# Performance work log

Measured on AMD Instinct MI355X. Metric: run time of the kernel, lower is better.

Reference implementation:

```python
import jax, jax.numpy as jnp
import numpy as np

B, H, W, C = 8, 64, 64, 256
EPS = 1e-5


def unfold(img, k, p):
    # img: [B, C, Hh, Ww] -> patches [B, C, k*k, Hh*Ww] (torch.nn.Unfold layout)
    b, c, hh, ww = img.shape
    xp = jnp.pad(img, ((0, 0), (0, 0), (p, p), (p, p)))
    pats = jnp.stack([xp[:, :, i:i + hh, j:j + ww]
                      for i in range(k) for j in range(k)], axis=2)
    return pats.reshape(b, c, k * k, hh * ww)


def fold(cols, k, p, hh, ww):
    # cols: [B, C*k*k, hh*ww] -> scatter-add back to [B, C, hh, ww] (torch.nn.Fold)
    b = cols.shape[0]
    c = cols.shape[1] // (k * k)
    pt = cols.reshape(b, c, k, k, hh, ww)
    out = jnp.zeros((b, c, hh + 2 * p, ww + 2 * p), cols.dtype)
    for i in range(k):
        for j in range(k):
            out = out.at[:, :, i:i + hh, j:j + ww].add(pt[:, :, i, j])
    return out[:, :, p:p + hh, p:p + ww]


def maxpool(img, k, p):
    # same-size max pool, stride 1
    return jax.lax.reduce_window(img, -jnp.inf, jax.lax.max,
                                 (1, 1, k, k), (1, 1, 1, 1),
                                 [(0, 0), (0, 0), (p, p), (p, p)])


def setup_inputs() -> dict:
    key = jax.random.key(0)
    ks = jax.random.split(key, 4)
    x = jax.random.normal(ks[0], (B, H, W, C), dtype=jnp.float32)
    Wv = jax.random.normal(ks[1], (C, C), dtype=jnp.float32) * 0.02
    bv = jnp.zeros((C,), jnp.float32)
    Wa = jax.random.normal(ks[2], (C, 81), dtype=jnp.float32) * 0.02
    ba = jnp.zeros((81,), jnp.float32)
    Wfu = jax.random.normal(ks[3], (2 * C, C), dtype=jnp.float32) * 0.02
    bfu = jnp.zeros((C,), jnp.float32)
    gamma = jnp.ones((C,), jnp.float32)
    beta = jnp.zeros((C,), jnp.float32)
    return {"x": x, "Wv": Wv, "bv": bv, "Wa": Wa, "ba": ba,
            "Wfu": Wfu, "bfu": bfu, "gamma": gamma, "beta": beta}


def reference(x, Wv, bv, Wa, ba, Wfu, bfu, gamma, beta):
    b, h, w, c = x.shape
    x3 = x
    # 3x3 windowed attention branch (5x5 branch in source is dead code: its
    # result is overwritten by `x2 = relu(x)` before use).
    v = x @ Wv + bv                                # [B,H,W,C]
    v_img = jnp.transpose(v, (0, 3, 2, 1))         # [B,C,W,H] (H/W swap as in source)
    pats = unfold(v_img, 3, 1)                     # [B,C,9,W*H]
    v3 = jnp.transpose(pats, (0, 3, 2, 1))         # [B,HW,9,C]
    a = (x @ Wa + ba).reshape(b, h * w, 9, 9)
    a = jax.nn.softmax(a, axis=-1)
    y = jnp.einsum('lbpq,lbqc->lbpc'.replace('l', 'n'), a, v3)  # [B,HW,9,C]
    y = jnp.transpose(y, (0, 3, 2, 1)).reshape(b, c * 9, h * w)
    xf = fold(y, 3, 1, h, w)                       # [B,C,H,W]
    xf = jnp.transpose(xf, (0, 3, 2, 1))           # [B,W,H,C]
    xr = jax.nn.relu(xf)
    x_max = jnp.transpose(x3, (0, 3, 2, 1))        # [B,C,W,H]
    m1 = jnp.transpose(maxpool(x_max, 3, 1), (0, 3, 2, 1))  # [B,H,W,C]
    x1 = jax.nn.relu(xr + m1)
    x2 = jax.nn.relu(x1)
    m2 = jnp.transpose(maxpool(x_max, 5, 2), (0, 3, 2, 1))
    x2 = jax.nn.relu(x2 + m2)
    xfu = jnp.concatenate([x1, x2], axis=-1) @ Wfu + bfu
    xfu = jax.nn.relu(xfu)
    out = x3 + xfu                                 # [B,H,W,C]
    # BatchNorm2d (training mode: batch stats) applied on [B,C,W,H]
    img = jnp.transpose(out, (0, 3, 2, 1))
    mean = img.mean(axis=(0, 2, 3), keepdims=True)
    var = img.var(axis=(0, 2, 3), keepdims=True)
    imgn = (img - mean) * jax.lax.rsqrt(var + EPS)
    imgn = imgn * gamma[None, :, None, None] + beta[None, :, None, None]
    return jnp.transpose(imgn, (0, 2, 3, 1))       # [B,W,H,C]
```

## Files before the change

kernel.cpp:

```cpp
#include <hip/hip_runtime.h>
#include <math.h>

#define NLOC 32768
#define CH 256

typedef __attribute__((ext_vector_type(8))) short short8;
typedef __attribute__((ext_vector_type(4))) float floatx4;

__device__ inline unsigned short f2bf(float x) {
  union { float f; unsigned u; } c; c.f = x;
  unsigned r = c.u + 0x7FFFu + ((c.u >> 16) & 1u);
  return (unsigned short)(r >> 16);
}
__device__ inline float bflo(unsigned u) {
  union { unsigned u; float f; } c; c.u = u << 16; return c.f;
}
__device__ inline float bfhi(unsigned u) {
  union { unsigned u; float f; } c; c.u = u & 0xFFFF0000u; return c.f;
}

__device__ __forceinline__ void gl_lds16(const void* g, void* l) {
  __builtin_amdgcn_global_load_lds(
      (const __attribute__((address_space(1))) unsigned int*)g,
      (__attribute__((address_space(3))) unsigned int*)l, 16, 0, 0);
}

__global__ __launch_bounds__(64) void k_pack_w(
    const float* __restrict__ Wv, const float* __restrict__ Wa,
    const float* __restrict__ Wfu, unsigned short* __restrict__ wp) {
  int fid = blockIdx.x;
  int l = threadIdx.x;
  const float* W; int ldn, nvalid, nf, ks;
  if (fid < 128)      { W = Wv;  ldn = 256; nvalid = 256; nf = fid >> 3; ks = fid & 7; }
  else if (fid < 384) { int f = fid - 128; W = Wfu; ldn = 256; nvalid = 256; nf = f >> 4; ks = f & 15; }
  else                { int f = fid - 384; W = Wa;  ldn = 81;  nvalid = 81;  nf = f >> 3; ks = f & 7; }
  unsigned short* dst = wp + (size_t)fid * 512;
  int c = nf * 16 + (l & 15);
  int k0 = ks * 32 + (l >> 4) * 8;
  unsigned short u[8];
#pragma unroll
  for (int j = 0; j < 8; ++j)
    u[j] = (c < nvalid) ? f2bf(W[(size_t)(k0 + j) * ldn + c]) : (unsigned short)0;
  uint4 pk;
  pk.x = u[0] | ((unsigned)u[1] << 16);
  pk.y = u[2] | ((unsigned)u[3] << 16);
  pk.z = u[4] | ((unsigned)u[5] << 16);
  pk.w = u[6] | ((unsigned)u[7] << 16);
  *(uint4*)(dst + l * 8) = pk;
}

__global__ __launch_bounds__(256) void k_pool(
    const float* __restrict__ x, unsigned short* __restrict__ rm3,
    unsigned short* __restrict__ rm5, unsigned short* __restrict__ xb) {
  int tid = threadIdx.x;
  int loc = blockIdx.x * 4 + (tid >> 6);
  int beta = loc & 63;
  int c0 = (tid & 63) * 4;
  const float* base = x + ((size_t)loc - beta) * CH + c0;
  const float NI = -INFINITY;
  float4 r3 = {NI, NI, NI, NI}, r5, xv;
#pragma unroll
  for (int d = -1; d <= 1; ++d) {
    int bb = beta + d;
    if ((unsigned)bb >= 64u) continue;
    float4 f = *(const float4*)(base + (size_t)bb * CH);
    if (d == 0) xv = f;
    r3.x = fmaxf(r3.x, f.x); r3.y = fmaxf(r3.y, f.y);
    r3.z = fmaxf(r3.z, f.z); r3.w = fmaxf(r3.w, f.w);
  }
  r5 = r3;
#pragma unroll
  for (int d = -2; d <= 2; d += 4) {
    int bb = beta + d;
    if ((unsigned)bb >= 64u) continue;
    float4 f = *(const float4*)(base + (size_t)bb * CH);
    r5.x = fmaxf(r5.x, f.x); r5.y = fmaxf(r5.y, f.y);
    r5.z = fmaxf(r5.z, f.z); r5.w = fmaxf(r5.w, f.w);
  }
  size_t o = (size_t)loc * CH + c0;
  uint2 p3, p5, px;
  p3.x = f2bf(r3.x) | ((unsigned)f2bf(r3.y) << 16);
  p3.y = f2bf(r3.z) | ((unsigned)f2bf(r3.w) << 16);
  p5.x = f2bf(r5.x) | ((unsigned)f2bf(r5.y) << 16);
  p5.y = f2bf(r5.z) | ((unsigned)f2bf(r5.w) << 16);
  px.x = f2bf(xv.x) | ((unsigned)f2bf(xv.y) << 16);
  px.y = f2bf(xv.z) | ((unsigned)f2bf(xv.w) << 16);
  *(uint2*)(rm3 + o) = p3;
  *(uint2*)(rm5 + o) = p5;
  *(uint2*)(xb + o) = px;
}

__global__ __launch_bounds__(256) void k_gemm_v(
    const unsigned short* __restrict__ xb, const unsigned short* __restrict__ wvp,
    const float* __restrict__ bv, unsigned short* __restrict__ v) {
  __shared__ unsigned short sA[16 * 512];
  __shared__ unsigned short sB[16 * 512];
  int tid = threadIdx.x, lane = tid & 63, w = tid >> 6;
  int r0 = (blockIdx.x >> 1) * 128;
  int nc0 = (blockIdx.x & 1) * 128;
  int mh = w >> 1, nq = w & 1;
  floatx4 acc[4][4];
#pragma unroll
  for (int mt = 0; mt < 4; ++mt)
#pragma unroll
    for (int nf = 0; nf < 4; ++nf) acc[mt][nf] = (floatx4)(0.f);
  for (int kt = 0; kt < 4; ++kt) {
    int kk = kt * 64;
#pragma unroll
    for (int f = 0; f < 4; ++f) {
      int fa = w * 4 + f;
      int mt = fa >> 1, ks = fa & 1;
      const unsigned short* g = xb + (size_t)(r0 + mt * 16 + (lane & 15)) * CH
                                + kk + ks * 32 + (lane >> 4) * 8;
      gl_lds16(g, &sA[fa * 512]);
    }
#pragma unroll
    for (int f = 0; f < 4; ++f) {
      int fb = w * 4 + f;
      int nf = fb >> 1, ks = fb & 1;
      int nfg = (nc0 >> 4) + nf;
      int ksg = kt * 2 + ks;
      const unsigned short* g = wvp + ((size_t)nfg * 8 + ksg) * 512 + lane * 8;
      gl_lds16(g, &sB[fb * 512]);
    }
    __syncthreads();
#pragma unroll
    for (int ks = 0; ks < 2; ++ks) {
      short8 af[4], bf[4];
#pragma unroll
      for (int mt = 0; mt < 4; ++mt)
        af[mt] = *(const short8*)&sA[(((mh * 4 + mt) << 1) + ks) * 512 + lane * 8];
#pragma unroll
      for (int nf = 0; nf < 4; ++nf)
        bf[nf] = *(const short8*)&sB[(((nq * 4 + nf) << 1) + ks) * 512 + lane * 8];
#pragma unroll
      for (int mt = 0; mt < 4; ++mt)
#pragma unroll
        for (int nf = 0; nf < 4; ++nf)
          acc[mt][nf] = __builtin_amdgcn_mfma_f32_16x16x32_bf16(af[mt], bf[nf], acc[mt][nf], 0, 0, 0);
    }
    if (kt < 3) __syncthreads();
  }
#pragma unroll
  for (int nf = 0; nf < 4; ++nf) {
    int c = nc0 + nq * 64 + nf * 16 + (lane & 15);
    float bb = bv[c];
#pragma unroll
    for (int mt = 0; mt < 4; ++mt) {
      int crow = r0 + mh * 64 + mt * 16 + (lane >> 4) * 4;
#pragma unroll
      for (int i = 0; i < 4; ++i)
        v[(size_t)(crow + i) * CH + c] = f2bf(acc[mt][nf][i] + bb);
    }
  }
}

__global__ __launch_bounds__(256) void k_gemm_a(
    const unsigned short* __restrict__ xb, const unsigned short* __restrict__ wap,
    const float* __restrict__ ba, float* __restrict__ A) {
  __shared__ float lg[64][96];
  int tid = threadIdx.x, lane = tid & 63, w = tid >> 6;
  int mtile = blockIdx.x * 4 + w;
  int r0 = mtile * 16;
  floatx4 acc[6];
#pragma unroll
  for (int i = 0; i < 6; ++i) acc[i] = (floatx4)(0.f);
  const unsigned short* abase = xb + (size_t)(r0 + (lane & 15)) * CH + (lane >> 4) * 8;
  for (int ks = 0; ks < 8; ++ks) {
    short8 af = *(const short8*)(abase + ks * 32);
#pragma unroll
    for (int nf = 0; nf < 6; ++nf) {
      short8 bfr = *(const short8*)(wap + ((size_t)(nf * 8) + ks) * 512 + lane * 8);
      acc[nf] = __builtin_amdgcn_mfma_f32_16x16x32_bf16(af, bfr, acc[nf], 0, 0, 0);
    }
  }
  int lrow = w * 16 + (lane >> 4) * 4;
#pragma unroll
  for (int nf = 0; nf < 6; ++nf) {
    int c = nf * 16 + (lane & 15);
    float bb = (c < 81) ? ba[c] : 0.f;
#pragma unroll
    for (int i = 0; i < 4; ++i)
      lg[lrow + i][c] = acc[nf][i] + bb;
  }
  __syncthreads();
  int loc0 = blockIdx.x * 64;
  for (int it = 0; it < 3; ++it) {
    int idx = tid + it * 256;
    if (idx < 576) {
      int row = idx / 9, g = idx % 9;
      float vals[9];
#pragma unroll
      for (int q = 0; q < 9; ++q) vals[q] = lg[row][g * 9 + q];
      float m = vals[0];
#pragma unroll
      for (int q = 1; q < 9; ++q) m = fmaxf(m, vals[q]);
      float s = 0.f;
#pragma unroll
      for (int q = 0; q < 9; ++q) { vals[q] = __expf(vals[q] - m); s += vals[q]; }
      float inv = 1.f / s;
      float* o = A + (size_t)(loc0 + row) * 81 + g * 9;
#pragma unroll
      for (int q = 0; q < 9; ++q) o[q] = vals[q] * inv;
    }
  }
}

__global__ __launch_bounds__(256) void k_attn(
    const float* __restrict__ A, const unsigned short* __restrict__ v,
    const unsigned short* __restrict__ rm3, const unsigned short* __restrict__ rm5,
    unsigned short* __restrict__ cat) {
  __shared__ unsigned short vs[5 * 12 * CH];
  __shared__ float w5_s[8][25];
  float* a_sf = (float*)vs;
  int tid = threadIdx.x;
  int loc0 = blockIdx.x * 8;
  int b = loc0 >> 12, alpha = (loc0 >> 6) & 63, beta0 = loc0 & 63;
  for (int idx = tid; idx < 8 * 81; idx += 256) {
    int li = idx / 81, t = idx - li * 81;
    int ij = t / 9, i = ij / 3, j = ij % 3;
    int lh = beta0 + li + 1 - i;
    int lw = alpha + 1 - j;
    float val = 0.f;
    if ((unsigned)lh < 64u && (unsigned)lw < 64u)
      val = A[(size_t)(b * 4096 + lh * 64 + lw) * 81 + t];
    a_sf[li * 81 + t] = val;
  }
  __syncthreads();
  for (int idx = tid; idx < 200; idx += 256) {
    int li = idx / 25, o = idx - li * 25;
    int dh = o / 5 - 2, dw = o % 5 - 2;
    float s = 0.f;
    int jlo = dh < 0 ? -dh : 0, jhi = dh > 0 ? 2 - dh : 2;
    int ilo = dw < 0 ? -dw : 0, ihi = dw > 0 ? 2 - dw : 2;
    for (int j = jlo; j <= jhi; ++j)
      for (int i = ilo; i <= ihi; ++i)
        s += a_sf[li * 81 + (i * 3 + j) * 9 + ((i + dw) * 3 + (j + dh))];
    w5_s[li][o] = s;
  }
  __syncthreads();
  const unsigned short* vb = v + (size_t)b * 4096 * CH;
  for (int i = tid; i < 1920; i += 256) {
    int row = i / 384, rem = i - row * 384, col = rem >> 5, ch8 = rem & 31;
    int hv = alpha - 2 + row, wv = beta0 - 2 + col;
    uint4 val = {0u, 0u, 0u, 0u};
    if ((unsigned)hv < 64u && (unsigned)wv < 64u)
      val = *(const uint4*)(vb + (size_t)(hv * 64 + wv) * CH + ch8 * 8);
    *(uint4*)(vs + (size_t)(row * 12 + col) * CH + ch8 * 8) = val;
  }
  __syncthreads();
  int li = tid >> 5, tc = tid & 31, c0 = tc * 8;
  int beta = beta0 + li;
  float m1[8], m2[8];
#pragma unroll
  for (int q = 0; q < 8; ++q) { m1[q] = -INFINITY; m2[q] = -INFINITY; }
#pragma unroll
  for (int da = -2; da <= 2; ++da) {
    int aa = alpha + da;
    if ((unsigned)aa >= 64u) continue;
    size_t ro = (size_t)((b * 64 + aa) * 64 + beta) * CH + c0;
    uint4 p5 = *(const uint4*)(rm5 + ro);
    m2[0] = fmaxf(m2[0], bflo(p5.x)); m2[1] = fmaxf(m2[1], bfhi(p5.x));
    m2[2] = fmaxf(m2[2], bflo(p5.y)); m2[3] = fmaxf(m2[3], bfhi(p5.y));
    m2[4] = fmaxf(m2[4], bflo(p5.z)); m2[5] = fmaxf(m2[5], bfhi(p5.z));
    m2[6] = fmaxf(m2[6], bflo(p5.w)); m2[7] = fmaxf(m2[7], bfhi(p5.w));
    if (da >= -1 && da <= 1) {
      uint4 p3 = *(const uint4*)(rm3 + ro);
      m1[0] = fmaxf(m1[0], bflo(p3.x)); m1[1] = fmaxf(m1[1], bfhi(p3.x));
      m1[2] = fmaxf(m1[2], bflo(p3.y)); m1[3] = fmaxf(m1[3], bfhi(p3.y));
      m1[4] = fmaxf(m1[4], bflo(p3.z)); m1[5] = fmaxf(m1[5], bfhi(p3.z));
      m1[6] = fmaxf(m1[6], bflo(p3.w)); m1[7] = fmaxf(m1[7], bfhi(p3.w));
    }
  }
  float acc[8];
#pragma unroll
  for (int q = 0; q < 8; ++q) acc[q] = 0.f;
#pragma unroll
  for (int dh = 0; dh < 5; ++dh) {
#pragma unroll
    for (int dw = 0; dw < 5; ++dw) {
      float wgt = w5_s[li][dh * 5 + dw];
      uint4 pk = *(const uint4*)(vs + (size_t)(dh * 12 + li + dw) * CH + c0);
      acc[0] = fmaf(wgt, bflo(pk.x), acc[0]);
      acc[1] = fmaf(wgt, bfhi(pk.x), acc[1]);
      acc[2] = fmaf(wgt, bflo(pk.y), acc[2]);
      acc[3] = fmaf(wgt, bfhi(pk.y), acc[3]);
      acc[4] = fmaf(wgt, bflo(pk.z), acc[4]);
      acc[5] = fmaf(wgt, bfhi(pk.z), acc[5]);
      acc[6] = fmaf(wgt, bflo(pk.w), acc[6]);
      acc[7] = fmaf(wgt, bfhi(pk.w), acc[7]);
    }
  }
  unsigned short u1[8], u2[8];
#pragma unroll
  for (int q = 0; q < 8; ++q) {
    float x1v = fmaxf(fmaxf(acc[q], 0.f) + m1[q], 0.f);
    float x2v = fmaxf(x1v + m2[q], 0.f);
    u1[q] = f2bf(x1v);
    u2[q] = f2bf(x2v);
  }
  unsigned short* cp = cat + (size_t)(loc0 + li) * 512 + c0;
  uint4 pk1, pk2;
  pk1.x = u1[0] | ((unsigned)u1[1] << 16); pk1.y = u1[2] | ((unsigned)u1[3] << 16);
  pk1.z = u1[4] | ((unsigned)u1[5] << 16); pk1.w = u1[6] | ((unsigned)u1[7] << 16);
  pk2.x = u2[0] | ((unsigned)u2[1] << 16); pk2.y = u2[2] | ((unsigned)u2[3] << 16);
  pk2.z = u2[4] | ((unsigned)u2[5] << 16); pk2.w = u2[6] | ((unsigned)u2[7] << 16);
  *(uint4*)(cp) = pk1;
  *(uint4*)(cp + 256) = pk2;
}

__global__ __launch_bounds__(256) void k_fuse(
    const float* __restrict__ x, const unsigned short* __restrict__ cat,
    const unsigned short* __restrict__ wfp, const float* __restrict__ bfu,
    float* __restrict__ outp, float* __restrict__ sums16) {
  __shared__ unsigned short sA[16 * 512];
  __shared__ unsigned short sB[16 * 512];
  __shared__ float bsum[512];
  int tid = threadIdx.x, lane = tid & 63, w = tid >> 6;
  for (int i = tid; i < 512; i += 256) bsum[i] = 0.f;
  int r0 = (blockIdx.x >> 1) * 128;
  int nc0 = (blockIdx.x & 1) * 128;
  int mh = w >> 1, nq = w & 1;
  floatx4 acc[4][4];
#pragma unroll
  for (int mt = 0; mt < 4; ++mt)
#pragma unroll
    for (int nf = 0; nf < 4; ++nf) acc[mt][nf] = (floatx4)(0.f);
  for (int kt = 0; kt < 8; ++kt) {
    int kk = kt * 64;
#pragma unroll
    for (int f = 0; f < 4; ++f) {
      int fa = w * 4 + f;
      int mt = fa >> 1, ks = fa & 1;
      const unsigned short* g = cat + (size_t)(r0 + mt * 16 + (lane & 15)) * 512
                                + kk + ks * 32 + (lane >> 4) * 8;
      gl_lds16(g, &sA[fa * 512]);
    }
#pragma unroll
    for (int f = 0; f < 4; ++f) {
      int fb = w * 4 + f;
      int nf = fb >> 1, ks = fb & 1;
      int nfg = (nc0 >> 4) + nf;
      int ksg = kt * 2 + ks;
      const unsigned short* g = wfp + ((size_t)nfg * 16 + ksg) * 512 + lane * 8;
      gl_lds16(g, &sB[fb * 512]);
    }
    __syncthreads();
#pragma unroll
    for (int ks = 0; ks < 2; ++ks) {
      short8 af[4], bf[4];
#pragma unroll
      for (int mt = 0; mt < 4; ++mt)
        af[mt] = *(const short8*)&sA[(((mh * 4 + mt) << 1) + ks) * 512 + lane * 8];
#pragma unroll
      for (int nf = 0; nf < 4; ++nf)
        bf[nf] = *(const short8*)&sB[(((nq * 4 + nf) << 1) + ks) * 512 + lane * 8];
#pragma unroll
      for (int mt = 0; mt < 4; ++mt)
#pragma unroll
        for (int nf = 0; nf < 4; ++nf)
          acc[mt][nf] = __builtin_amdgcn_mfma_f32_16x16x32_bf16(af[mt], bf[nf], acc[mt][nf], 0, 0, 0);
    }
    if (kt < 7) __syncthreads();
  }
#pragma unroll
  for (int nf = 0; nf < 4; ++nf) {
    int c = nc0 + nq * 64 + nf * 16 + (lane & 15);
    float bb = bfu[c];
    float s = 0.f, ss = 0.f;
#pragma unroll
    for (int mt = 0; mt < 4; ++mt) {
      int crow = r0 + mh * 64 + mt * 16 + (lane >> 4) * 4;
#pragma unroll
      for (int i = 0; i < 4; ++i) {
        int r = crow + i;
        float xv = x[(size_t)r * CH + c];
        float o = xv + fmaxf(acc[mt][nf][i] + bb, 0.f);
        int b_ = r >> 12, al = (r >> 6) & 63, be = r & 63;
        outp[((size_t)(b_ * 64 + be) * 64 + al) * CH + c] = o;
        s += o; ss += o * o;
      }
    }
    s += __shfl_xor(s, 16);  s += __shfl_xor(s, 32);
    ss += __shfl_xor(ss, 16); ss += __shfl_xor(ss, 32);
    if (lane < 16) {
      atomicAdd(&bsum[c & 255], s);
      atomicAdd(&bsum[256 + (c & 255)], ss);
    }
  }
  __syncthreads();
  float* bank = sums16 + (size_t)(blockIdx.x & 15) * 512;
  for (int i = tid; i < 512; i += 256) atomicAdd(&bank[i], bsum[i]);
}

__global__ void k_bnprep(const float* __restrict__ sums16,
                         const float* __restrict__ gamma,
                         const float* __restrict__ beta_,
                         float* __restrict__ sc) {
  int c = threadIdx.x;
  float s = 0.f, ss = 0.f;
#pragma unroll
  for (int bk = 0; bk < 16; ++bk) {
    s += sums16[(size_t)bk * 512 + c];
    ss += sums16[(size_t)bk * 512 + 256 + c];
  }
  const float inv_n = 1.f / (float)NLOC;
  float mean = s * inv_n;
  float var = ss * inv_n - mean * mean;
  float scale = gamma[c] * rsqrtf(var + 1e-5f);
  sc[c] = scale;
  sc[256 + c] = beta_[c] - mean * scale;
}

__global__ __launch_bounds__(256) void k_bn(
    float* __restrict__ outp, const float* __restrict__ sc, int n4) {
  __shared__ float s[512];
  const int tid = threadIdx.x;
  for (int i = tid; i < 512; i += 256) s[i] = sc[i];
  __syncthreads();
  for (int i = blockIdx.x * 256 + tid; i < n4; i += gridDim.x * 256) {
    float4 val = ((float4*)outp)[i];
    int c0 = (i & 63) * 4;
    val.x = val.x * s[c0 + 0] + s[256 + c0 + 0];
    val.y = val.y * s[c0 + 1] + s[256 + c0 + 1];
    val.z = val.z * s[c0 + 2] + s[256 + c0 + 2];
    val.w = val.w * s[c0 + 3] + s[256 + c0 + 3];
    ((float4*)outp)[i] = val;
  }
}

extern "C" void kernel_launch(void* const* d_in, const int* in_sizes, int n_in,
                              void* d_out, int out_size, void* d_ws, size_t ws_size,
                              hipStream_t stream) {
  const float* x     = (const float*)d_in[0];
  const float* Wv    = (const float*)d_in[1];
  const float* bv    = (const float*)d_in[2];
  const float* Wa    = (const float*)d_in[3];
  const float* ba    = (const float*)d_in[4];
  const float* Wfu   = (const float*)d_in[5];
  const float* bfu   = (const float*)d_in[6];
  const float* gamma = (const float*)d_in[7];
  const float* beta_ = (const float*)d_in[8];
  float* out = (float*)d_out;

  float* sums16 = (float*)d_ws;
  float* sc   = sums16 + 16 * 512;
  unsigned short* wp   = (unsigned short*)(sc + 512);
  unsigned short* wvp  = wp;
  unsigned short* wfp  = wp + (size_t)128 * 512;
  unsigned short* wap  = wp + (size_t)384 * 512;
  unsigned short* vbuf = wp + (size_t)432 * 512;
  float* Abuf = (float*)(vbuf + (size_t)NLOC * CH);
  unsigned short* cat = (unsigned short*)(Abuf + (size_t)NLOC * 81);
  unsigned short* rm3 = cat + (size_t)NLOC * 512;
  unsigned short* rm5 = rm3 + (size_t)NLOC * CH;
  unsigned short* xb  = rm5 + (size_t)NLOC * CH;

  hipMemsetAsync(sums16, 0, 16 * 512 * sizeof(float), stream);

  k_pack_w<<<432, 64, 0, stream>>>(Wv, Wa, Wfu, wp);
  k_pool<<<8192, 256, 0, stream>>>(x, rm3, rm5, xb);
  k_gemm_v<<<512, 256, 0, stream>>>(xb, wvp, bv, vbuf);
  k_gemm_a<<<512, 256, 0, stream>>>(xb, wap, ba, Abuf);
  k_attn<<<4096, 256, 0, stream>>>(Abuf, vbuf, rm3, rm5, cat);
  k_fuse<<<512, 256, 0, stream>>>(x, cat, wfp, bfu, out, sums16);
  k_bnprep<<<1, 256, 0, stream>>>(sums16, gamma, beta_, sc);
  k_bn<<<2048, 256, 0, stream>>>(out, sc, NLOC * CH / 4);
}
```

Measured before the change: 131.7 us.

## Double-buffer LDS tiles in both GEMMs and widen attention blocks to 512 threads

Both bf16 MFMA GEMM kernels now keep two LDS stages and issue the global-to-LDS loads for the next K tile before computing on the current one, so load latency can overlap with the MFMA work. LDS use per block doubles, which may lower occupancy. Separately, the attention kernel runs with 512 threads per block, each handling 4 channels instead of 8, to give more parallelism per location. This halves the width of each vector access and adds more threads to the staging loops.

```diff
diff --git a/kernel.cpp b/kernel.cpp
--- a/kernel.cpp
+++ b/kernel.cpp
@@ -93,8 +93,8 @@
 __global__ __launch_bounds__(256) void k_gemm_v(
     const unsigned short* __restrict__ xb, const unsigned short* __restrict__ wvp,
     const float* __restrict__ bv, unsigned short* __restrict__ v) {
-  __shared__ unsigned short sA[16 * 512];
-  __shared__ unsigned short sB[16 * 512];
+  __shared__ unsigned short sA[2][16 * 512];
+  __shared__ unsigned short sB[2][16 * 512];
   int tid = threadIdx.x, lane = tid & 63, w = tid >> 6;
   int r0 = (blockIdx.x >> 1) * 128;
   int nc0 = (blockIdx.x & 1) * 128;
@@ -104,42 +104,46 @@
   for (int mt = 0; mt < 4; ++mt)
 #pragma unroll
     for (int nf = 0; nf < 4; ++nf) acc[mt][nf] = (floatx4)(0.f);
+#pragma unroll
+  for (int f = 0; f < 4; ++f) {
+    int fa = w * 4 + f, mt = fa >> 1, ks = fa & 1;
+    gl_lds16(xb + (size_t)(r0 + mt * 16 + (lane & 15)) * CH + ks * 32 + (lane >> 4) * 8,
+             &sA[0][fa * 512]);
+    int fb = fa, nf = fb >> 1;
+    gl_lds16(wvp + ((size_t)((nc0 >> 4) + nf) * 8 + ks) * 512 + lane * 8,
+             &sB[0][fb * 512]);
+  }
+  __syncthreads();
   for (int kt = 0; kt < 4; ++kt) {
-    int kk = kt * 64;
-#pragma unroll
-    for (int f = 0; f < 4; ++f) {
-      int fa = w * 4 + f;
-      int mt = fa >> 1, ks = fa & 1;
-      const unsigned short* g = xb + (size_t)(r0 + mt * 16 + (lane & 15)) * CH
-                                + kk + ks * 32 + (lane >> 4) * 8;
-      gl_lds16(g, &sA[fa * 512]);
-    }
-#pragma unroll
-    for (int f = 0; f < 4; ++f) {
-      int fb = w * 4 + f;
-      int nf = fb >> 1, ks = fb & 1;
-      int nfg = (nc0 >> 4) + nf;
-      int ksg = kt * 2 + ks;
-      const unsigned short* g = wvp + ((size_t)nfg * 8 + ksg) * 512 + lane * 8;
-      gl_lds16(g, &sB[fb * 512]);
-    }
-    __syncthreads();
+    int cur = kt & 1;
+    if (kt < 3) {
+      int kn = kt + 1, nb = kn & 1, kkn = kn * 64;
+#pragma unroll
+      for (int f = 0; f < 4; ++f) {
+        int fa = w * 4 + f, mt = fa >> 1, ks = fa & 1;
+        gl_lds16(xb + (size_t)(r0 + mt * 16 + (lane & 15)) * CH + kkn + ks * 32 + (lane >> 4) * 8,
+                 &sA[nb][fa * 512]);
+        int fb = fa, nf = fb >> 1;
+        gl_lds16(wvp + ((size_t)((nc0 >> 4) + nf) * 8 + kn * 2 + ks) * 512 + lane * 8,
+                 &sB[nb][fb * 512]);
+      }
+    }
 #pragma unroll
     for (int ks = 0; ks < 2; ++ks) {
       short8 af[4], bf[4];
 #pragma unroll
       for (int mt = 0; mt < 4; ++mt)
-        af[mt] = *(const short8*)&sA[(((mh * 4 + mt) << 1) + ks) * 512 + lane * 8];
+        af[mt] = *(const short8*)&sA[cur][(((mh * 4 + mt) << 1) + ks) * 512 + lane * 8];
 #pragma unroll
       for (int nf = 0; nf < 4; ++nf)
-        bf[nf] = *(const short8*)&sB[(((nq * 4 + nf) << 1) + ks) * 512 + lane * 8];
+        bf[nf] = *(const short8*)&sB[cur][(((nq * 4 + nf) << 1) + ks) * 512 + lane * 8];
 #pragma unroll
       for (int mt = 0; mt < 4; ++mt)
 #pragma unroll
         for (int nf = 0; nf < 4; ++nf)
           acc[mt][nf] = __builtin_amdgcn_mfma_f32_16x16x32_bf16(af[mt], bf[nf], acc[mt][nf], 0, 0, 0);
     }
-    if (kt < 3) __syncthreads();
+    __syncthreads();
   }
 #pragma unroll
   for (int nf = 0; nf < 4; ++nf) {
@@ -206,7 +210,7 @@
   }
 }
 
-__global__ __launch_bounds__(256) void k_attn(
+__global__ __launch_bounds__(512) void k_attn(
     const float* __restrict__ A, const unsigned short* __restrict__ v,
     const unsigned short* __restrict__ rm3, const unsigned short* __restrict__ rm5,
     unsigned short* __restrict__ cat) {
@@ -216,7 +220,7 @@
   int tid = threadIdx.x;
   int loc0 = blockIdx.x * 8;
   int b = loc0 >> 12, alpha = (loc0 >> 6) & 63, beta0 = loc0 & 63;
-  for (int idx = tid; idx < 8 * 81; idx += 256) {
+  for (int idx = tid; idx < 8 * 81; idx += 512) {
     int li = idx / 81, t = idx - li * 81;
     int ij = t / 9, i = ij / 3, j = ij % 3;
     int lh = beta0 + li + 1 - i;
@@ -227,8 +231,8 @@
     a_sf[li * 81 + t] = val;
   }
   __syncthreads();
-  for (int idx = tid; idx < 200; idx += 256) {
-    int li = idx / 25, o = idx - li * 25;
+  if (tid < 200) {
+    int li = tid / 25, o = tid - li * 25;
     int dh = o / 5 - 2, dw = o % 5 - 2;
     float s = 0.f;
     int jlo = dh < 0 ? -dh : 0, jhi = dh > 0 ? 2 - dh : 2;
@@ -240,7 +244,7 @@
   }
   __syncthreads();
   const unsigned short* vb = v + (size_t)b * 4096 * CH;
-  for (int i = tid; i < 1920; i += 256) {
+  for (int i = tid; i < 1920; i += 512) {
     int row = i / 384, rem = i - row * 384, col = rem >> 5, ch8 = rem & 31;
     int hv = alpha - 2 + row, wv = beta0 - 2 + col;
     uint4 val = {0u, 0u, 0u, 0u};
@@ -249,72 +253,60 @@
     *(uint4*)(vs + (size_t)(row * 12 + col) * CH + ch8 * 8) = val;
   }
   __syncthreads();
-  int li = tid >> 5, tc = tid & 31, c0 = tc * 8;
+  int li = tid >> 6, tc = tid & 63, c0 = tc * 4;
   int beta = beta0 + li;
-  float m1[8], m2[8];
-#pragma unroll
-  for (int q = 0; q < 8; ++q) { m1[q] = -INFINITY; m2[q] = -INFINITY; }
+  float m1[4], m2[4];
+#pragma unroll
+  for (int q = 0; q < 4; ++q) { m1[q] = -INFINITY; m2[q] = -INFINITY; }
 #pragma unroll
   for (int da = -2; da <= 2; ++da) {
     int aa = alpha + da;
     if ((unsigned)aa >= 64u) continue;
     size_t ro = (size_t)((b * 64 + aa) * 64 + beta) * CH + c0;
-    uint4 p5 = *(const uint4*)(rm5 + ro);
+    uint2 p5 = *(const uint2*)(rm5 + ro);
     m2[0] = fmaxf(m2[0], bflo(p5.x)); m2[1] = fmaxf(m2[1], bfhi(p5.x));
     m2[2] = fmaxf(m2[2], bflo(p5.y)); m2[3] = fmaxf(m2[3], bfhi(p5.y));
-    m2[4] = fmaxf(m2[4], bflo(p5.z)); m2[5] = fmaxf(m2[5], bfhi(p5.z));
-    m2[6] = fmaxf(m2[6], bflo(p5.w)); m2[7] = fmaxf(m2[7], bfhi(p5.w));
     if (da >= -1 && da <= 1) {
-      uint4 p3 = *(const uint4*)(rm3 + ro);
+      uint2 p3 = *(const uint2*)(rm3 + ro);
       m1[0] = fmaxf(m1[0], bflo(p3.x)); m1[1] = fmaxf(m1[1], bfhi(p3.x));
       m1[2] = fmaxf(m1[2], bflo(p3.y)); m1[3] = fmaxf(m1[3], bfhi(p3.y));
-      m1[4] = fmaxf(m1[4], bflo(p3.z)); m1[5] = fmaxf(m1[5], bfhi(p3.z));
-      m1[6] = fmaxf(m1[6], bflo(p3.w)); m1[7] = fmaxf(m1[7], bfhi(p3.w));
-    }
-  }
-  float acc[8];
-#pragma unroll
-  for (int q = 0; q < 8; ++q) acc[q] = 0.f;
+    }
+  }
+  float acc[4] = {0.f, 0.f, 0.f, 0.f};
 #pragma unroll
   for (int dh = 0; dh < 5; ++dh) {
 #pragma unroll
     for (int dw = 0; dw < 5; ++dw) {
       float wgt = w5_s[li][dh * 5 + dw];
-      uint4 pk = *(const uint4*)(vs + (size_t)(dh * 12 + li + dw) * CH + c0);
+      uint2 pk = *(const uint2*)(vs + (size_t)(dh * 12 + li + dw) * CH + c0);
       acc[0] = fmaf(wgt, bflo(pk.x), acc[0]);
       acc[1] = fmaf(wgt, bfhi(pk.x), acc[1]);
       acc[2] = fmaf(wgt, bflo(pk.y), acc[2]);
       acc[3] = fmaf(wgt, bfhi(pk.y), acc[3]);
-      acc[4] = fmaf(wgt, bflo(pk.z), acc[4]);
-      acc[5] = fmaf(wgt, bfhi(pk.z), acc[5]);
-      acc[6] = fmaf(wgt, bflo(pk.w), acc[6]);
-      acc[7] = fmaf(wgt, bfhi(pk.w), acc[7]);
-    }
-  }
-  unsigned short u1[8], u2[8];
-#pragma unroll
-  for (int q = 0; q < 8; ++q) {
+    }
+  }
+  unsigned short u1[4], u2[4];
+#pragma unroll
+  for (int q = 0; q < 4; ++q) {
     float x1v = fmaxf(fmaxf(acc[q], 0.f) + m1[q], 0.f);
     float x2v = fmaxf(x1v + m2[q], 0.f);
     u1[q] = f2bf(x1v);
     u2[q] = f2bf(x2v);
   }
   unsigned short* cp = cat + (size_t)(loc0 + li) * 512 + c0;
-  uint4 pk1, pk2;
+  uint2 pk1, pk2;
   pk1.x = u1[0] | ((unsigned)u1[1] << 16); pk1.y = u1[2] | ((unsigned)u1[3] << 16);
-  pk1.z = u1[4] | ((unsigned)u1[5] << 16); pk1.w = u1[6] | ((unsigned)u1[7] << 16);
   pk2.x = u2[0] | ((unsigned)u2[1] << 16); pk2.y = u2[2] | ((unsigned)u2[3] << 16);
-  pk2.z = u2[4] | ((unsigned)u2[5] << 16); pk2.w = u2[6] | ((unsigned)u2[7] << 16);
-  *(uint4*)(cp) = pk1;
-  *(uint4*)(cp + 256) = pk2;
+  *(uint2*)(cp) = pk1;
+  *(uint2*)(cp + 256) = pk2;
 }
 
 __global__ __launch_bounds__(256) void k_fuse(
     const float* __restrict__ x, const unsigned short* __restrict__ cat,
     const unsigned short* __restrict__ wfp, const float* __restrict__ bfu,
     float* __restrict__ outp, float* __restrict__ sums16) {
-  __shared__ unsigned short sA[16 * 512];
-  __shared__ unsigned short sB[16 * 512];
+  __shared__ unsigned short sA[2][16 * 512];
+  __shared__ unsigned short sB[2][16 * 512];
   __shared__ float bsum[512];
   int tid = threadIdx.x, lane = tid & 63, w = tid >> 6;
   for (int i = tid; i < 512; i += 256) bsum[i] = 0.f;
@@ -326,42 +318,46 @@
   for (int mt = 0; mt < 4; ++mt)
 #pragma unroll
     for (int nf = 0; nf < 4; ++nf) acc[mt][nf] = (floatx4)(0.f);
+#pragma unroll
+  for (int f = 0; f < 4; ++f) {
+    int fa = w * 4 + f, mt = fa >> 1, ks = fa & 1;
+    gl_lds16(cat + (size_t)(r0 + mt * 16 + (lane & 15)) * 512 + ks * 32 + (lane >> 4) * 8,
+             &sA[0][fa * 512]);
+    int nf = fa >> 1;
+    gl_lds16(wfp + ((size_t)((nc0 >> 4) + nf) * 16 + ks) * 512 + lane * 8,
+             &sB[0][fa * 512]);
+  }
+  __syncthreads();
   for (int kt = 0; kt < 8; ++kt) {
-    int kk = kt * 64;
-#pragma unroll
-    for (int f = 0; f < 4; ++f) {
-      int fa = w * 4 + f;
-      int mt = fa >> 1, ks = fa & 1;
-      const unsigned short* g = cat + (size_t)(r0 + mt * 16 + (lane & 15)) * 512
-                                + kk + ks * 32 + (lane >> 4) * 8;
-      gl_lds16(g, &sA[fa * 512]);
-    }
-#pragma unroll
-    for (int f = 0; f < 4; ++f) {
-      int fb = w * 4 + f;
-      int nf = fb >> 1, ks = fb & 1;
-      int nfg = (nc0 >> 4) + nf;
-      int ksg = kt * 2 + ks;
-      const unsigned short* g = wfp + ((size_t)nfg * 16 + ksg) * 512 + lane * 8;
-      gl_lds16(g, &sB[fb * 512]);
-    }
-    __syncthreads();
+    int cur = kt & 1;
+    if (kt < 7) {
+      int kn = kt + 1, nb = kn & 1, kkn = kn * 64;
+#pragma unroll
+      for (int f = 0; f < 4; ++f) {
+        int fa = w * 4 + f, mt = fa >> 1, ks = fa & 1;
+        gl_lds16(cat + (size_t)(r0 + mt * 16 + (lane & 15)) * 512 + kkn + ks * 32 + (lane >> 4) * 8,
+                 &sA[nb][fa * 512]);
+        int nf = fa >> 1;
+        gl_lds16(wfp + ((size_t)((nc0 >> 4) + nf) * 16 + kn * 2 + ks) * 512 + lane * 8,
+                 &sB[nb][fa * 512]);
+      }
+    }
 #pragma unroll
     for (int ks = 0; ks < 2; ++ks) {
       short8 af[4], bf[4];
 #pragma unroll
       for (int mt = 0; mt < 4; ++mt)
-        af[mt] = *(const short8*)&sA[(((mh * 4 + mt) << 1) + ks) * 512 + lane * 8];
+        af[mt] = *(const short8*)&sA[cur][(((mh * 4 + mt) << 1) + ks) * 512 + lane * 8];
 #pragma unroll
       for (int nf = 0; nf < 4; ++nf)
-        bf[nf] = *(const short8*)&sB[(((nq * 4 + nf) << 1) + ks) * 512 + lane * 8];
+        bf[nf] = *(const short8*)&sB[cur][(((nq * 4 + nf) << 1) + ks) * 512 + lane * 8];
 #pragma unroll
       for (int mt = 0; mt < 4; ++mt)
 #pragma unroll
         for (int nf = 0; nf < 4; ++nf)
           acc[mt][nf] = __builtin_amdgcn_mfma_f32_16x16x32_bf16(af[mt], bf[nf], acc[mt][nf], 0, 0, 0);
     }
-    if (kt < 7) __syncthreads();
+    __syncthreads();
   }
 #pragma unroll
   for (int nf = 0; nf < 4; ++nf) {
@@ -462,7 +458,7 @@
   k_pool<<<8192, 256, 0, stream>>>(x, rm3, rm5, xb);
   k_gemm_v<<<512, 256, 0, stream>>>(xb, wvp, bv, vbuf);
   k_gemm_a<<<512, 256, 0, stream>>>(xb, wap, ba, Abuf);
-  k_attn<<<4096, 256, 0, stream>>>(Abuf, vbuf, rm3, rm5, cat);
+  k_attn<<<4096, 512, 0, stream>>>(Abuf, vbuf, rm3, rm5, cat);
   k_fuse<<<512, 256, 0, stream>>>(x, cat, wfp, bfu, out, sums16);
   k_bnprep<<<1, 256, 0, stream>>>(sums16, gamma, beta_, sc);
   k_bn<<<2048, 256, 0, stream>>>(out, sc, NLOC * CH / 4);
```

After: 132.7 us. About the same (+0.8%).
